# Performance work log

Hardware: AMD Instinct MI355X
Metric: run time of the kernel (lower is better)

The kernel has to match this reference:

```python
import jax, jax.numpy as jnp
import numpy as np

K = 3           # kernel_size
PAD = 1         # padding
HEADS = 6
C = 192
CH = C // HEADS           # channels per head = 32
SCALE = CH ** (-0.5)
KK = K * K                # 9


def unfold3(x):
    # x: [N,C,H,W] -> [N,C,9,H,W] (im2col with k=3, pad=1, stride=1)
    N, c, H, W = x.shape
    xp = jnp.pad(x, ((0, 0), (0, 0), (PAD, PAD), (PAD, PAD)))
    return jnp.stack([xp[:, :, i:i + H, j:j + W] for i in range(K) for j in range(K)], axis=2)


def fold3(y):
    # y: [N,C,9,H,W] -> [N,C,H,W] (scatter-add inverse of unfold3)
    N, c, kk, H, W = y.shape
    out = jnp.zeros((N, c, H + 2 * PAD, W + 2 * PAD), dtype=y.dtype)
    idx = 0
    for i in range(K):
        for j in range(K):
            out = out.at[:, :, i:i + H, j:j + W].add(y[:, :, idx])
            idx += 1
    return out[:, :, PAD:PAD + H, PAD:PAD + W]


def setup_inputs() -> dict:
    key = jax.random.key(0)
    ks = jax.random.split(key, 6)
    N, H, W = 16, 56, 56
    s = 0.02
    return {
        "x": jax.random.normal(ks[0], (N, C, H, W), jnp.float32),
        "Wv": jax.random.normal(ks[1], (C, C), jnp.float32) * s,          # fc (no bias)
        "Wa": jax.random.normal(ks[2], (C, KK * KK * HEADS), jnp.float32) * s,  # fc_att weight
        "ba": jax.random.normal(ks[3], (KK * KK * HEADS,), jnp.float32) * s,
        "Wp": jax.random.normal(ks[4], (C, C), jnp.float32) * s,          # fc_proj weight
        "bp": jax.random.normal(ks[5], (C,), jnp.float32) * s,
    }


def reference(x, Wv, Wa, ba, Wp, bp):
    N, c, H, W = x.shape
    HW = H * W
    # value projection (pointwise linear over channels)
    v = jnp.einsum("nchw,cd->ndhw", x, Wv)
    # unfold values: [N,C,9,H,W] -> [N,heads,ch,9,HW] -> [N,heads,HW,9,ch]
    vu = unfold3(v).reshape(N, HEADS, CH, KK, HW).transpose(0, 1, 4, 3, 2)
    # attention logits from (avg-pooled, here identity since stride=1) input
    att = jnp.einsum("nchw,ck->nhwk", x, Wa) + ba       # [N,H,W,81*heads]
    att = att.reshape(N, HW, HEADS, KK, KK).transpose(0, 2, 1, 3, 4)  # [N,heads,HW,9,9]
    att = jax.nn.softmax(att * SCALE, axis=-1)          # dropout is identity at inference
    # apply per-position 9x9 attention to the 9 gathered neighbors
    out = jnp.einsum("nhpkl,nhplc->nhpkc", att, vu)      # [N,heads,HW,9,ch]
    # fold back: layout (heads, ch, kk) matches unfold layout (C, kk)
    out = out.transpose(0, 1, 4, 3, 2).reshape(N, c, KK, H, W)
    folded = fold3(out)                                  # [N,C,H,W]
    # output projection
    return jnp.einsum("nchw,cd->ndhw", folded, Wp) + bp[None, :, None, None]
```

## Files before the change

### kernel.cpp

```cpp
#include <hip/hip_runtime.h>
#include <hip/hip_bf16.h>
#include <math.h>

#define HW 3136
#define NPOS 50176
#define NC 192
#define NHEADS 6
#define IMG 56
#define NATT 486
#define ATT_SCALE 0.17677669529663687f

typedef __attribute__((ext_vector_type(8))) short short8;
typedef __attribute__((ext_vector_type(8))) unsigned short ushort8;
typedef __attribute__((ext_vector_type(4))) float float4v;
typedef __attribute__((ext_vector_type(4))) unsigned int uint4v;

__device__ __forceinline__ float bf2f(unsigned short u) {
    unsigned int x = ((unsigned int)u) << 16;
    return __builtin_bit_cast(float, x);
}
__device__ __forceinline__ float bf2f_lo(unsigned int u) {
    return __builtin_bit_cast(float, u << 16);
}
__device__ __forceinline__ float bf2f_hi(unsigned int u) {
    return __builtin_bit_cast(float, u & 0xffff0000u);
}
__device__ __forceinline__ unsigned short f2bf(float f) {
    __hip_bfloat16 h = __float2bfloat16(f);
    return __builtin_bit_cast(unsigned short, h);
}
__device__ __forceinline__ void gload_lds16(const void* g, void* l) {
    __builtin_amdgcn_global_load_lds((const __attribute__((address_space(1))) void*)g,
                                     (__attribute__((address_space(3))) void*)l, 16, 0, 0);
}

__global__ __launch_bounds__(256) void transpose_x(const float* __restrict__ x,
                                                   unsigned short* __restrict__ xt)
{
    __shared__ float tile[64][65];
    int bx = blockIdx.x;
    int n = (bx * 64) / HW;
    int hw0 = (bx * 64) % HW;
    int c0 = blockIdx.y * 64;
    int tl = threadIdx.x & 63, tg = threadIdx.x >> 6;
    const float* xn = x + (size_t)n * NC * HW;
#pragma unroll
    for (int i = 0; i < 16; ++i)
        tile[tg * 16 + i][tl] = xn[(size_t)(c0 + tg * 16 + i) * HW + hw0 + tl];
    __syncthreads();
    unsigned short* xp = xt + ((size_t)n * HW + hw0) * NC + c0;
#pragma unroll
    for (int i = 0; i < 16; ++i) {
        int hwr = tg * 16 + i;
        xp[(size_t)hwr * NC + tl] = f2bf(tile[tl][hwr]);
    }
}

__global__ __launch_bounds__(256) void prep_weights(
    const float* __restrict__ Wv, const float* __restrict__ Wa, const float* __restrict__ Wp,
    const float* __restrict__ ba,
    unsigned short* __restrict__ Wall, unsigned short* __restrict__ Wpt,
    float* __restrict__ ball)
{
    int idx = blockIdx.x * 256 + threadIdx.x;
    if (idx < 36864) {
        int d = idx / 192, k = idx - d * 192;
        Wpt[idx] = f2bf(Wp[(size_t)k * NC + d]);
    }
    if (idx < 147456) {
        int d = idx / 192, k = idx - d * 192;
        unsigned short val;
        float bv = 0.f;
        if (d < 192) {
            val = f2bf(Wv[(size_t)k * NC + d]);
        } else {
            int dp = d - 192;
            int head = dp / 96, rr = dp - head * 96;
            int k9 = rr / 10, l = rr - k9 * 10;
            bool valid = (k9 < 9) && (l < 9);
            int src = head * 81 + k9 * 9 + l;
            val = valid ? f2bf(Wa[(size_t)k * NATT + src]) : (unsigned short)0;
            bv = valid ? ba[src] : 0.f;
        }
        Wall[idx] = val;
        if (k == 0) ball[d] = bv;
    }
}

__global__ __launch_bounds__(256) void gemm_big(
    const unsigned short* __restrict__ A, const unsigned short* __restrict__ W,
    const float* __restrict__ ball,
    unsigned short* __restrict__ Vo, unsigned short* __restrict__ ATo)
{
    __shared__ __align__(16) unsigned short As[2][4096];
    __shared__ __align__(16) unsigned short Bs[2][4096];
    int t = threadIdx.x, lane = t & 63, wave = t >> 6;
    int bi = blockIdx.x;
    int slot = bi >> 3;
    int q6 = slot / 6;
    int rr_ = (bi & 7) + 8 * q6;
    int cc_ = slot - 6 * q6;
    int col0 = cc_ * 128, row0 = rr_ * 128;
    int fr = lane & 15, fq = lane >> 4;
    int wm = (wave >> 1) * 64, wn = (wave & 1) * 64;
    int srow = lane >> 2;
    int soff = (lane & 3) * 16;
    const char* Ab = (const char*)A;
    const char* Wb = (const char*)W;

    float4v acc[4][4] = {};

#define STAGE_BIG(buf, k0)                                                        \
    {                                                                             \
        _Pragma("unroll")                                                         \
        for (int i = 0; i < 2; ++i) {                                             \
            int j = wave * 2 + i;                                                 \
            gload_lds16(Ab + (size_t)(row0 + j * 16 + srow) * 384 + (k0)*2 + soff,\
                        (char*)As[buf] + j * 1024);                               \
            gload_lds16(Wb + (size_t)(col0 + j * 16 + srow) * 384 + (k0)*2 + soff,\
                        (char*)Bs[buf] + j * 1024);                               \
        }                                                                         \
    }

    STAGE_BIG(0, 0);
    for (int s = 0; s < 6; ++s) {
        if (s < 5) {
            STAGE_BIG((s + 1) & 1, (s + 1) * 32);
            asm volatile("s_waitcnt vmcnt(4)\n\ts_barrier" ::: "memory");
        } else {
            asm volatile("s_waitcnt vmcnt(0)\n\ts_barrier" ::: "memory");
        }
        int buf = s & 1;
        short8 af[4], bf[4];
#pragma unroll
        for (int mi = 0; mi < 4; ++mi)
            af[mi] = *(const short8*)((const char*)As[buf] + (wm + mi * 16 + fr) * 64 + fq * 16);
#pragma unroll
        for (int ni = 0; ni < 4; ++ni)
            bf[ni] = *(const short8*)((const char*)Bs[buf] + (wn + ni * 16 + fr) * 64 + fq * 16);
        asm volatile("s_waitcnt lgkmcnt(0)\n\ts_barrier" ::: "memory");
#pragma unroll
        for (int mi = 0; mi < 4; ++mi)
#pragma unroll
            for (int ni = 0; ni < 4; ++ni)
                acc[mi][ni] = __builtin_amdgcn_mfma_f32_16x16x32_bf16(
                    af[mi], bf[ni], acc[mi][ni], 0, 0, 0);
    }

#pragma unroll
    for (int ni = 0; ni < 4; ++ni) {
        int col = col0 + wn + ni * 16 + fr;
        float b = ball[col];
        unsigned short* bptr;
        size_t rstr;
        bool valid;
        if (col < 192) {
            int hd = col >> 5, ch = col & 31;
            bptr = Vo + ((size_t)hd * NPOS) * 32 + ch;
            rstr = 32;
            valid = true;
        } else {
            int dp = col - 192;
            int hd = dp / 96, rr = dp - hd * 96;
            int k9 = rr / 10, l = rr - k9 * 10;
            valid = (k9 < 9);
            bptr = ATo + ((size_t)(hd * 9 + (k9 < 9 ? k9 : 8)) * NPOS) * 10 + l;
            rstr = 10;
        }
#pragma unroll
        for (int mi = 0; mi < 4; ++mi) {
            int row = row0 + wm + mi * 16 + fq * 4;
#pragma unroll
            for (int r = 0; r < 4; ++r) {
                unsigned short val = f2bf(acc[mi][ni][r] + b);
                if (valid) bptr[(size_t)(row + r) * rstr] = val;
            }
        }
    }
#undef STAGE_BIG
}

__global__ __launch_bounds__(256) void gemm_small(
    const unsigned short* __restrict__ A,
    const unsigned short* __restrict__ B,
    const float* __restrict__ bias, float* __restrict__ out)
{
    __shared__ __align__(16) unsigned short As[2][2048];
    __shared__ __align__(16) unsigned short Bs[2][8192];
    int t = threadIdx.x, lane = t & 63, wave = t >> 6;
    int n0 = blockIdx.x * 256, m0 = blockIdx.y * 64;
    int fr = lane & 15, fq = lane >> 4;
    int srow = lane >> 2, soff = (lane & 3) * 16;
    const char* Ab = (const char*)A;
    const char* Bb = (const char*)B;

    float4v acc[4][4] = {};

#define STAGE_SMALL(buf, k0)                                                      \
    {                                                                             \
        gload_lds16(Ab + (size_t)(m0 + wave * 16 + srow) * 384 + (k0)*2 + soff,   \
                    (char*)As[buf] + wave * 1024);                                \
        _Pragma("unroll")                                                         \
        for (int i = 0; i < 4; ++i) {                                             \
            int j = wave * 4 + i;                                                 \
            gload_lds16(Bb + (size_t)(n0 + j * 16 + srow) * 384 + (k0)*2 + soff,  \
                        (char*)Bs[buf] + j * 1024);                               \
        }                                                                         \
    }

    STAGE_SMALL(0, 0);
    for (int s = 0; s < 6; ++s) {
        if (s < 5) {
            STAGE_SMALL((s + 1) & 1, (s + 1) * 32);
            asm volatile("s_waitcnt vmcnt(5)\n\ts_barrier" ::: "memory");
        } else {
            asm volatile("s_waitcnt vmcnt(0)\n\ts_barrier" ::: "memory");
        }
        int buf = s & 1;
        short8 af[4], bf[4];
#pragma unroll
        for (int mi = 0; mi < 4; ++mi)
            af[mi] = *(const short8*)((const char*)As[buf] + (mi * 16 + fr) * 64 + fq * 16);
#pragma unroll
        for (int ni = 0; ni < 4; ++ni)
            bf[ni] = *(const short8*)((const char*)Bs[buf] + (wave * 64 + ni * 16 + fr) * 64 + fq * 16);
        asm volatile("s_waitcnt lgkmcnt(0)\n\ts_barrier" ::: "memory");
#pragma unroll
        for (int mi = 0; mi < 4; ++mi)
#pragma unroll
            for (int ni = 0; ni < 4; ++ni)
                acc[mi][ni] = __builtin_amdgcn_mfma_f32_16x16x32_bf16(
                    af[mi], bf[ni], acc[mi][ni], 0, 0, 0);
    }

#pragma unroll
    for (int ni = 0; ni < 4; ++ni) {
        int n = n0 + wave * 64 + ni * 16 + fr;
        int img = n / HW, phw = n - img * HW;
        float* op = out + (size_t)img * (NC * HW) + phw;
#pragma unroll
        for (int mi = 0; mi < 4; ++mi) {
            int m = m0 + mi * 16 + fq * 4;
#pragma unroll
            for (int r = 0; r < 4; ++r)
                op[(size_t)(m + r) * HW] = acc[mi][ni][r] + bias[m + r];
        }
    }
#undef STAGE_SMALL
}

__global__ __launch_bounds__(256, 4) void fused_att_agg(
    const unsigned short* __restrict__ V, const unsigned short* __restrict__ AT,
    unsigned short* __restrict__ fold)
{
    __shared__ __align__(16) char vt[4 * 434 * 16];
    int t = threadIdx.x;
    int bid = blockIdx.x;
    int head = bid % NHEADS; int tmp = bid / NHEADS;
    int tcol = tmp & 1; tmp >>= 1;
    int trow = tmp % 7; int img = tmp / 7;
    int h0 = trow * 8, w0 = tcol * 28;

    const unsigned short* Vh = V + (size_t)head * NPOS * 32;
    ushort8 stg[6];
#pragma unroll
    for (int i = 0; i < 6; ++i) {
        int u = i * 256 + t;
        int slot = u >> 2, q = u & 3;
        int vrow = slot >> 5, vcol = slot & 31;
        int hh = h0 - 2 + vrow, ww = w0 - 2 + vcol;
        bool ok = (hh >= 0) & (hh < IMG) & (ww >= 0) & (ww < IMG);
        int hc = min(max(hh, 0), IMG - 1);
        int wcl = min(max(ww, 0), IMG - 1);
        ushort8 val = *(const ushort8*)(Vh + (size_t)(img * HW + hc * IMG + wcl) * 32 + q * 8);
        if (!ok) val = (ushort8){};
        stg[i] = val;
    }

    int ph = t / 28, pw = t - (t / 28) * 28;
    int h = h0 + ph, w = w0 + pw;
    float wc[25];
#pragma unroll
    for (int d = 0; d < 25; ++d) wc[d] = 0.f;
    if (t < 224) {
        int head9 = head * 9;
#pragma unroll
        for (int k = 0; k < 9; ++k) {
            const int oky = k / 3 - 1, okx = k % 3 - 1;
            int hh = h - oky, ww = w - okx;
            bool ok = (hh >= 0) & (hh < IMG) & (ww >= 0) & (ww < IMG);
            int hc = min(max(hh, 0), IMG - 1);
            int wcl = min(max(ww, 0), IMG - 1);
            size_t nidx = (size_t)img * HW + hc * IMG + wcl;
            const unsigned int* ap32 =
                (const unsigned int*)(AT + ((size_t)(head9 + k) * NPOS + nidx) * 10);
            unsigned int u0 = ap32[0], u1 = ap32[1], u2 = ap32[2], u3 = ap32[3], u4 = ap32[4];
            float a[9] = { bf2f_lo(u0), bf2f_hi(u0), bf2f_lo(u1), bf2f_hi(u1),
                           bf2f_lo(u2), bf2f_hi(u2), bf2f_lo(u3), bf2f_hi(u3),
                           bf2f_lo(u4) };
            float m = -1e30f;
#pragma unroll
            for (int l = 0; l < 9; ++l) m = fmaxf(m, a[l]);
            float s = 0.f;
#pragma unroll
            for (int l = 0; l < 9; ++l) {
                a[l] = __expf((a[l] - m) * ATT_SCALE);
                s += a[l];
            }
            float g = ok ? (1.f / s) : 0.f;
#pragma unroll
            for (int l = 0; l < 9; ++l) {
                const int dy = (l / 3 - 1) - oky + 2;
                const int dx = (l % 3 - 1) - okx + 2;
                wc[dy * 5 + dx] += a[l] * g;
            }
        }
    }

#pragma unroll
    for (int i = 0; i < 6; ++i) {
        int u = i * 256 + t;
        int slot = u >> 2, q = u & 3;
        int vrow = slot >> 5, vcol = slot & 31;
        *(ushort8*)(vt + q * (434 * 16) + (vrow * 36 + vcol) * 16) = stg[i];
    }
    __syncthreads();

    if (t < 224) {
        int base = (ph * 36 + pw) * 16;
        int pos = img * HW + h * IMG + w;
        unsigned short* fo = fold + (size_t)pos * NC + head * 32;
#pragma unroll
        for (int q = 0; q < 4; ++q) {
            const char* vq = vt + q * (434 * 16) + base;
            float acc[8];
#pragma unroll
            for (int j = 0; j < 8; ++j) acc[j] = 0.f;
#pragma unroll
            for (int d = 0; d < 25; ++d) {
                const int dy = d / 5, dx = d % 5;
                float wf = wc[d];
                uint4v vv = *(const uint4v*)(vq + (dy * 36 + dx) * 16);
#pragma unroll
                for (int z = 0; z < 4; ++z) {
                    acc[2 * z]     += wf * bf2f_lo(vv[z]);
                    acc[2 * z + 1] += wf * bf2f_hi(vv[z]);
                }
            }
            ushort8 ov;
#pragma unroll
            for (int j = 0; j < 8; ++j) ov[j] = f2bf(acc[j]);
            *(ushort8*)(fo + q * 8) = ov;
        }
    }
}

extern "C" void kernel_launch(void* const* d_in, const int* in_sizes, int n_in,
                              void* d_out, int out_size, void* d_ws, size_t ws_size,
                              hipStream_t stream)
{
    const float* x  = (const float*)d_in[0];
    const float* Wv = (const float*)d_in[1];
    const float* Wa = (const float*)d_in[2];
    const float* ba = (const float*)d_in[3];
    const float* Wp = (const float*)d_in[4];
    const float* bp = (const float*)d_in[5];
    float* out = (float*)d_out;

    unsigned short* xt   = (unsigned short*)d_ws;
    unsigned short* V    = xt + 9633792;
    unsigned short* AT   = V + 9633792;
    unsigned short* Wall = AT + 27095040;
    unsigned short* Wpt  = Wall + 147456;
    float*          ball = (float*)(Wpt + 36864);
    unsigned short* foldb = xt;

    dim3 blk(256);
    prep_weights<<<576, blk, 0, stream>>>(Wv, Wa, Wp, ba, Wall, Wpt, ball);
    transpose_x<<<dim3(784, 3), blk, 0, stream>>>(x, xt);
    gemm_big<<<2352, blk, 0, stream>>>(xt, Wall, ball, V, AT);
    fused_att_agg<<<1344, blk, 0, stream>>>(V, AT, foldb);
    gemm_small<<<dim3(196, 3), blk, 0, stream>>>(Wpt, foldb, bp, out);
}
```

Baseline: 186.8 us.

## Load GEMM fragments directly from global memory instead of LDS staging

Both GEMM kernels drop the double-buffered global-to-LDS staging, along with its barriers, and have each wave load its MFMA fragments straight from global memory, with the K loop fully unrolled. The aim is to remove LDS round trips and barrier synchronisation, since K is only 192 and tiles are small. In exchange, data shared between waves is fetched redundantly from global memory or L2, and loads are 16-byte per-lane accesses strided by rows rather than cooperative coalesced staging.

```diff
diff --git a/kernel.cpp b/kernel.cpp
--- a/kernel.cpp
+++ b/kernel.cpp
@@ -28,10 +28,6 @@
 __device__ __forceinline__ unsigned short f2bf(float f) {
     __hip_bfloat16 h = __float2bfloat16(f);
     return __builtin_bit_cast(unsigned short, h);
-}
-__device__ __forceinline__ void gload_lds16(const void* g, void* l) {
-    __builtin_amdgcn_global_load_lds((const __attribute__((address_space(1))) void*)g,
-                                     (__attribute__((address_space(3))) void*)l, 16, 0, 0);
 }
 
 __global__ __launch_bounds__(256) void transpose_x(const float* __restrict__ x,
@@ -92,8 +88,6 @@
     const float* __restrict__ ball,
     unsigned short* __restrict__ Vo, unsigned short* __restrict__ ATo)
 {
-    __shared__ __align__(16) unsigned short As[2][4096];
-    __shared__ __align__(16) unsigned short Bs[2][4096];
     int t = threadIdx.x, lane = t & 63, wave = t >> 6;
     int bi = blockIdx.x;
     int slot = bi >> 3;
@@ -103,42 +97,21 @@
     int col0 = cc_ * 128, row0 = rr_ * 128;
     int fr = lane & 15, fq = lane >> 4;
     int wm = (wave >> 1) * 64, wn = (wave & 1) * 64;
-    int srow = lane >> 2;
-    int soff = (lane & 3) * 16;
-    const char* Ab = (const char*)A;
-    const char* Wb = (const char*)W;
+
+    const char* pA = (const char*)A + (size_t)(row0 + wm + fr) * 384 + fq * 16;
+    const char* pB = (const char*)W + (size_t)(col0 + wn + fr) * 384 + fq * 16;
 
     float4v acc[4][4] = {};
 
-#define STAGE_BIG(buf, k0)                                                        \
-    {                                                                             \
-        _Pragma("unroll")                                                         \
-        for (int i = 0; i < 2; ++i) {                                             \
-            int j = wave * 2 + i;                                                 \
-            gload_lds16(Ab + (size_t)(row0 + j * 16 + srow) * 384 + (k0)*2 + soff,\
-                        (char*)As[buf] + j * 1024);                               \
-            gload_lds16(Wb + (size_t)(col0 + j * 16 + srow) * 384 + (k0)*2 + soff,\
-                        (char*)Bs[buf] + j * 1024);                               \
-        }                                                                         \
-    }
-
-    STAGE_BIG(0, 0);
+#pragma unroll
     for (int s = 0; s < 6; ++s) {
-        if (s < 5) {
-            STAGE_BIG((s + 1) & 1, (s + 1) * 32);
-            asm volatile("s_waitcnt vmcnt(4)\n\ts_barrier" ::: "memory");
-        } else {
-            asm volatile("s_waitcnt vmcnt(0)\n\ts_barrier" ::: "memory");
-        }
-        int buf = s & 1;
         short8 af[4], bf[4];
 #pragma unroll
         for (int mi = 0; mi < 4; ++mi)
-            af[mi] = *(const short8*)((const char*)As[buf] + (wm + mi * 16 + fr) * 64 + fq * 16);
+            af[mi] = *(const short8*)(pA + mi * (16 * 384) + s * 64);
 #pragma unroll
         for (int ni = 0; ni < 4; ++ni)
-            bf[ni] = *(const short8*)((const char*)Bs[buf] + (wn + ni * 16 + fr) * 64 + fq * 16);
-        asm volatile("s_waitcnt lgkmcnt(0)\n\ts_barrier" ::: "memory");
+            bf[ni] = *(const short8*)(pB + ni * (16 * 384) + s * 64);
 #pragma unroll
         for (int mi = 0; mi < 4; ++mi)
 #pragma unroll
@@ -177,7 +150,6 @@
             }
         }
     }
-#undef STAGE_BIG
 }
 
 __global__ __launch_bounds__(256) void gemm_small(
@@ -185,46 +157,24 @@
     const unsigned short* __restrict__ B,
     const float* __restrict__ bias, float* __restrict__ out)
 {
-    __shared__ __align__(16) unsigned short As[2][2048];
-    __shared__ __align__(16) unsigned short Bs[2][8192];
     int t = threadIdx.x, lane = t & 63, wave = t >> 6;
     int n0 = blockIdx.x * 256, m0 = blockIdx.y * 64;
     int fr = lane & 15, fq = lane >> 4;
-    int srow = lane >> 2, soff = (lane & 3) * 16;
-    const char* Ab = (const char*)A;
-    const char* Bb = (const char*)B;
+
+    const char* pA = (const char*)A + (size_t)(m0 + fr) * 384 + fq * 16;
+    const char* pB = (const char*)B + (size_t)(n0 + wave * 64 + fr) * 384 + fq * 16;
 
     float4v acc[4][4] = {};
 
-#define STAGE_SMALL(buf, k0)                                                      \
-    {                                                                             \
-        gload_lds16(Ab + (size_t)(m0 + wave * 16 + srow) * 384 + (k0)*2 + soff,   \
-                    (char*)As[buf] + wave * 1024);                                \
-        _Pragma("unroll")                                                         \
-        for (int i = 0; i < 4; ++i) {                                             \
-            int j = wave * 4 + i;                                                 \
-            gload_lds16(Bb + (size_t)(n0 + j * 16 + srow) * 384 + (k0)*2 + soff,  \
-                        (char*)Bs[buf] + j * 1024);                               \
-        }                                                                         \
-    }
-
-    STAGE_SMALL(0, 0);
+#pragma unroll
     for (int s = 0; s < 6; ++s) {
-        if (s < 5) {
-            STAGE_SMALL((s + 1) & 1, (s + 1) * 32);
-            asm volatile("s_waitcnt vmcnt(5)\n\ts_barrier" ::: "memory");
-        } else {
-            asm volatile("s_waitcnt vmcnt(0)\n\ts_barrier" ::: "memory");
-        }
-        int buf = s & 1;
         short8 af[4], bf[4];
 #pragma unroll
         for (int mi = 0; mi < 4; ++mi)
-            af[mi] = *(const short8*)((const char*)As[buf] + (mi * 16 + fr) * 64 + fq * 16);
+            af[mi] = *(const short8*)(pA + mi * (16 * 384) + s * 64);
 #pragma unroll
         for (int ni = 0; ni < 4; ++ni)
-            bf[ni] = *(const short8*)((const char*)Bs[buf] + (wave * 64 + ni * 16 + fr) * 64 + fq * 16);
-        asm volatile("s_waitcnt lgkmcnt(0)\n\ts_barrier" ::: "memory");
+            bf[ni] = *(const short8*)(pB + ni * (16 * 384) + s * 64);
 #pragma unroll
         for (int mi = 0; mi < 4; ++mi)
 #pragma unroll
@@ -246,7 +196,6 @@
                 op[(size_t)(m + r) * HW] = acc[mi][ni][r] + bias[m + r];
         }
     }
-#undef STAGE_SMALL
 }
 
 __global__ __launch_bounds__(256, 4) void fused_att_agg(
```

New measurement: 223.2 us. 19.5% more time.
